# Performance work log

Measured on AMD Instinct MI355X. Metric: run time of the kernel, lower is better.

The kernel has to match this reference:

```python
import jax, jax.numpy as jnp
import numpy as np

VOCAB = 50257
BATCH = 512
SEQ = 1024


def setup_inputs() -> dict:
    key = jax.random.key(0)
    kx, kidf = jax.random.split(key)
    x = jax.random.randint(kx, (BATCH, SEQ), 0, VOCAB, dtype=jnp.int64)
    # idf weights are positive; uniform in (0.1, 5.0) mimics real idf values
    idf = jax.random.uniform(kidf, (VOCAB,), dtype=jnp.float32, minval=0.1, maxval=5.0)
    return {"x": x, "idf": idf}


def reference(x, idf):
    B, S = x.shape
    V = idf.shape[0]
    # term-frequency histogram: scatter-add directly into (B, V) accumulator,
    # equivalent to the one-hot scatter_ + sum over seq in the original
    rows = jnp.arange(B, dtype=x.dtype)[:, None]           # (B, 1)
    tf = jnp.zeros((B, V), dtype=jnp.float32).at[rows, x].add(1.0)
    tfidf = tf * idf                                        # (B, V)
    n = jnp.sum(tfidf, axis=1, keepdims=True)               # (B, 1)
    return tfidf / n
```

## Files before the change

### kernel.cpp

```cpp
#include <hip/hip_runtime.h>


constexpr int VOCAB = 50257;
constexpr int SEQ = 1024;
constexpr int BATCH = 512;
constexpr int HWORDS = (VOCAB + 1) / 2;
constexpr int NTHREADS = 1024;

__global__ __launch_bounds__(NTHREADS)
void tfidf_kernel(const int* __restrict__ x,
                  const float* __restrict__ idf,
                  float* __restrict__ out) {
    __shared__ unsigned int cnt[HWORDS];
    __shared__ float red[NTHREADS / 64];
    __shared__ float s_inv_n;

    const int b   = blockIdx.x;
    const int tid = threadIdx.x;

    for (int i = tid; i < HWORDS; i += NTHREADS) cnt[i] = 0u;
    __syncthreads();

    const int tok = x[(size_t)b * SEQ + tid];
    atomicAdd(&cnt[tok >> 1], (tok & 1) ? 65536u : 1u);

    float v = idf[tok];
    #pragma unroll
    for (int off = 32; off > 0; off >>= 1) v += __shfl_down(v, off, 64);
    if ((tid & 63) == 0) red[tid >> 6] = v;
    __syncthreads();
    if (tid == 0) {
        float n = 0.0f;
        #pragma unroll
        for (int w = 0; w < NTHREADS / 64; ++w) n += red[w];
        s_inv_n = 1.0f / n;
    }
    __syncthreads();
    const float inv_n = s_inv_n;

    float* __restrict__ orow = out + (size_t)b * VOCAB;
    for (int vi = tid; vi < VOCAB; vi += NTHREADS) {
        const unsigned w = cnt[vi >> 1];
        const unsigned c = (vi & 1) ? (w >> 16) : (w & 0xffffu);
        orow[vi] = (float)c * idf[vi] * inv_n;
    }
}

extern "C" void kernel_launch(void* const* d_in, const int* in_sizes, int n_in,
                              void* d_out, int out_size, void* d_ws, size_t ws_size,
                              hipStream_t stream) {
    const int*   x   = (const int*)d_in[0];
    const float* idf = (const float*)d_in[1];
    float*       out = (float*)d_out;
    tfidf_kernel<<<dim3(BATCH), dim3(NTHREADS), 0, stream>>>(x, idf, out);
}
```

Measured before the change: 115.3 us.

## Replace shared-memory histogram with zero-fill plus global atomic scatter

The per-block 100KB shared-memory count histogram is dropped. Each row is now zero-filled with aligned float4 stores, with scalar head and tail handling for rows whose start is not 16-byte aligned. After the block-wide idf sum, each token atomically adds idf[tok]/n straight into the output. This removes the large LDS allocation that capped occupancy, the dense idf reads and the per-element scalar compute loop. The cost is 1024 global float atomics per row, and the float rounding for repeated tokens may differ slightly from count*idf.

```diff
diff --git a/kernel.cpp b/kernel.cpp
--- a/kernel.cpp
+++ b/kernel.cpp
@@ -4,27 +4,34 @@
 constexpr int VOCAB = 50257;
 constexpr int SEQ = 1024;
 constexpr int BATCH = 512;
-constexpr int HWORDS = (VOCAB + 1) / 2;
-constexpr int NTHREADS = 1024;
+constexpr int NT = 1024;
 
-__global__ __launch_bounds__(NTHREADS)
+__global__ __launch_bounds__(NT)
 void tfidf_kernel(const int* __restrict__ x,
                   const float* __restrict__ idf,
                   float* __restrict__ out) {
-    __shared__ unsigned int cnt[HWORDS];
-    __shared__ float red[NTHREADS / 64];
+    __shared__ float red[NT / 64];
     __shared__ float s_inv_n;
 
     const int b   = blockIdx.x;
     const int tid = threadIdx.x;
 
-    for (int i = tid; i < HWORDS; i += NTHREADS) cnt[i] = 0u;
-    __syncthreads();
+    const int   tok    = x[(size_t)b * SEQ + tid];
+    const float my_idf = idf[tok];
 
-    const int tok = x[(size_t)b * SEQ + tid];
-    atomicAdd(&cnt[tok >> 1], (tok & 1) ? 65536u : 1u);
+    float* __restrict__ orow = out + (size_t)b * VOCAB;
 
-    float v = idf[tok];
+    const int head = (4 - (b & 3)) & 3;
+    const int n4   = (VOCAB - head) >> 2;
+    const int tail = VOCAB - head - (n4 << 2);
+
+    if (tid < head) orow[tid] = 0.0f;
+    float4* __restrict__ p4 = (float4*)(orow + head);
+    const float4 z4 = make_float4(0.0f, 0.0f, 0.0f, 0.0f);
+    for (int c = tid; c < n4; c += NT) p4[c] = z4;
+    if (tid < tail) orow[head + (n4 << 2) + tid] = 0.0f;
+
+    float v = my_idf;
     #pragma unroll
     for (int off = 32; off > 0; off >>= 1) v += __shfl_down(v, off, 64);
     if ((tid & 63) == 0) red[tid >> 6] = v;
@@ -32,18 +39,12 @@
     if (tid == 0) {
         float n = 0.0f;
         #pragma unroll
-        for (int w = 0; w < NTHREADS / 64; ++w) n += red[w];
+        for (int w = 0; w < NT / 64; ++w) n += red[w];
         s_inv_n = 1.0f / n;
     }
     __syncthreads();
-    const float inv_n = s_inv_n;
 
-    float* __restrict__ orow = out + (size_t)b * VOCAB;
-    for (int vi = tid; vi < VOCAB; vi += NTHREADS) {
-        const unsigned w = cnt[vi >> 1];
-        const unsigned c = (vi & 1) ? (w >> 16) : (w & 0xffffu);
-        orow[vi] = (float)c * idf[vi] * inv_n;
-    }
+    atomicAdd(orow + tok, my_idf * s_inv_n);
 }
 
 extern "C" void kernel_launch(void* const* d_in, const int* in_sizes, int n_in,
@@ -52,5 +53,5 @@
     const int*   x   = (const int*)d_in[0];
     const float* idf = (const float*)d_in[1];
     float*       out = (float*)d_out;
-    tfidf_kernel<<<dim3(BATCH), dim3(NTHREADS), 0, stream>>>(x, idf, out);
+    tfidf_kernel<<<dim3(BATCH), dim3(NT), 0, stream>>>(x, idf, out);
 }
```

Result: slower. 128.1 us (+11.0%).
